# Kernel optimization log

Measured on AMD Instinct MI355X. Metric: run time of the kernel, lower is better.

The kernel has to match this reference:

```python
import jax, jax.numpy as jnp
import numpy as np

N_NODES = 50000


def _gcn_norm(edge_index):
    # symmetric GCN normalization 1/sqrt(deg_src*deg_dst), computed from edge list
    src, dst = edge_index[0], edge_index[1]
    ones = jnp.ones(src.shape[0], dtype=jnp.float32)
    deg = jax.ops.segment_sum(ones, dst, num_segments=N_NODES)
    deg = jnp.maximum(deg, 1.0)
    inv_sqrt = jax.lax.rsqrt(deg)
    return inv_sqrt[src] * inv_sqrt[dst]  # [E]


def _graph_conv(x, src, dst, norm, W, b):
    # gather messages from source nodes, normalize, scatter-add to destinations
    msgs = x[src] * norm[:, None]                       # [E, F]
    agg = jax.ops.segment_sum(msgs, dst, num_segments=N_NODES)  # [N, F]
    return agg @ W + b


def setup_inputs() -> dict:
    key = jax.random.key(0)
    ks = jax.random.split(key, 8)
    F, H, C, E = 128, 256, 40, 600000
    x = jax.random.normal(ks[0], (N_NODES, F), dtype=jnp.float32)
    edge_index = jax.random.randint(ks[1], (2, E), 0, N_NODES, dtype=jnp.int32)
    W1 = jax.random.normal(ks[2], (F, H), dtype=jnp.float32) * (1.0 / np.sqrt(F))
    b1 = jnp.zeros((H,), dtype=jnp.float32)
    W2 = jax.random.normal(ks[3], (H, H), dtype=jnp.float32) * (1.0 / np.sqrt(H))
    b2 = jnp.zeros((H,), dtype=jnp.float32)
    Wd = jax.random.normal(ks[4], (H, C), dtype=jnp.float32) * (1.0 / np.sqrt(H))
    bd = jnp.zeros((C,), dtype=jnp.float32)
    return {"x": x, "edge_index": edge_index, "W1": W1, "b1": b1,
            "W2": W2, "b2": b2, "Wd": Wd, "bd": bd}


def reference(x, edge_index, W1, b1, W2, b2, Wd, bd):
    src, dst = edge_index[0], edge_index[1]
    norm = _gcn_norm(edge_index)
    h = jax.nn.relu(_graph_conv(x, src, dst, norm, W1, b1))
    h = jax.nn.relu(_graph_conv(h, src, dst, norm, W2, b2))
    return jax.nn.softmax(h @ Wd + bd, axis=-1)
```

## Files before the change

kernel.cpp:

```cpp
#include <hip/hip_runtime.h>
#include <hip/hip_bf16.h>
#include <math.h>

#define N_NODES 50000

typedef short short8 __attribute__((ext_vector_type(8)));
typedef float f32x4 __attribute__((ext_vector_type(4)));

static __device__ __forceinline__ void split2(float x, unsigned short& hi, unsigned short& lo) {
    unsigned u = __builtin_bit_cast(unsigned, x);
    unsigned r = u + 0x7FFF + ((u >> 16) & 1);
    hi = (unsigned short)(r >> 16);
    float hf = __builtin_bit_cast(float, (unsigned)hi << 16);
    float res = x - hf;
    unsigned v = __builtin_bit_cast(unsigned, res);
    unsigned r2 = v + 0x7FFF + ((v >> 16) & 1);
    lo = (unsigned short)(r2 >> 16);
}


__global__ void deg_kernel(const int* __restrict__ dst, int* __restrict__ deg, int E) {
    int e = blockIdx.x * blockDim.x + threadIdx.x;
    if (e < E) atomicAdd(&deg[dst[e]], 1);
}


__global__ void scan_p1(const int* __restrict__ deg, int* __restrict__ bsum, int n) {
    int t = threadIdx.x;
    int base = blockIdx.x * 1024 + t * 4;
    int4 v = make_int4(0, 0, 0, 0);
    if (base + 3 < n) v = *(const int4*)(deg + base);
    else {
        if (base + 0 < n) v.x = deg[base + 0];
        if (base + 1 < n) v.y = deg[base + 1];
        if (base + 2 < n) v.z = deg[base + 2];
    }
    int s = v.x + v.y + v.z + v.w;
    #pragma unroll
    for (int off = 32; off > 0; off >>= 1) s += __shfl_xor(s, off);
    __shared__ int wpart[4];
    if ((t & 63) == 0) wpart[t >> 6] = s;
    __syncthreads();
    if (t == 0) bsum[blockIdx.x] = wpart[0] + wpart[1] + wpart[2] + wpart[3];
}

__global__ void scan_p2(int* __restrict__ bsum, int nb, int* __restrict__ rowptr, int n) {
    int t = threadIdx.x;
    int v = (t < nb) ? bsum[t] : 0;
    int sc = v;
    #pragma unroll
    for (int off = 1; off < 64; off <<= 1) {
        int u = __shfl_up(sc, off);
        if (t >= off) sc += u;
    }
    if (t < nb) bsum[t] = sc - v;
    if (t == 63) rowptr[n] = sc;
}

__global__ void scan_p3(const int* __restrict__ deg, const int* __restrict__ bsum,
                        int* __restrict__ rowptr, int* __restrict__ cursor,
                        float* __restrict__ inv, int n) {
    int t = threadIdx.x;
    int base = blockIdx.x * 1024 + t * 4;
    int4 v = make_int4(0, 0, 0, 0);
    if (base + 3 < n) v = *(const int4*)(deg + base);
    else {
        if (base + 0 < n) v.x = deg[base + 0];
        if (base + 1 < n) v.y = deg[base + 1];
        if (base + 2 < n) v.z = deg[base + 2];
    }
    int s = v.x + v.y + v.z + v.w;
    int lane = t & 63;
    int sc = s;
    #pragma unroll
    for (int off = 1; off < 64; off <<= 1) {
        int u = __shfl_up(sc, off);
        if (lane >= off) sc += u;
    }
    __shared__ int wpart[4], woff[4];
    if (lane == 63) wpart[t >> 6] = sc;
    __syncthreads();
    if (t == 0) { int a = 0; for (int i = 0; i < 4; ++i) { woff[i] = a; a += wpart[i]; } }
    __syncthreads();
    int run = bsum[blockIdx.x] + woff[t >> 6] + (sc - s);
    if (base + 0 < n) { rowptr[base + 0] = run; cursor[base + 0] = run; run += v.x; inv[base + 0] = rsqrtf(fmaxf((float)v.x, 1.0f)); }
    if (base + 1 < n) { rowptr[base + 1] = run; cursor[base + 1] = run; run += v.y; inv[base + 1] = rsqrtf(fmaxf((float)v.y, 1.0f)); }
    if (base + 2 < n) { rowptr[base + 2] = run; cursor[base + 2] = run; run += v.z; inv[base + 2] = rsqrtf(fmaxf((float)v.z, 1.0f)); }
    if (base + 3 < n) { rowptr[base + 3] = run; cursor[base + 3] = run; run += v.w; inv[base + 3] = rsqrtf(fmaxf((float)v.w, 1.0f)); }
}


__global__ void fill_kernel(const int* __restrict__ src, const int* __restrict__ dst,
                            const float* __restrict__ inv, int* __restrict__ cursor,
                            int* __restrict__ src_s, float* __restrict__ norm_s, int E) {
    int e = blockIdx.x * blockDim.x + threadIdx.x;
    if (e >= E) return;
    int s = src[e];
    int d = dst[e];
    int pos = atomicAdd(&cursor[d], 1);
    src_s[pos] = s;
    norm_s[pos] = inv[s] * inv[d];
}


__global__ void gather_agg_pass(const float* __restrict__ x, int coff, int ss,
                                const int* __restrict__ rowptr, const int* __restrict__ src_s,
                                const float* __restrict__ norm_s,
                                unsigned short* __restrict__ agg_hi,
                                unsigned short* __restrict__ agg_lo, int as) {
    int node = blockIdx.x * 4 + (threadIdx.x >> 6);
    if (node >= N_NODES) return;
    int lane = threadIdx.x & 63;
    int beg = rowptr[node];
    int end = rowptr[node + 1];
    const float* xb = x + coff + (size_t)lane * 2;

    float2 acc = {0.0f, 0.0f};
    int p = beg;
    for (; p + 4 <= end; p += 4) {
        int s0 = src_s[p], s1 = src_s[p + 1], s2 = src_s[p + 2], s3 = src_s[p + 3];
        float n0 = norm_s[p], n1 = norm_s[p + 1], n2 = norm_s[p + 2], n3 = norm_s[p + 3];
        float2 v0 = *(const float2*)(xb + (size_t)s0 * ss);
        float2 v1 = *(const float2*)(xb + (size_t)s1 * ss);
        float2 v2 = *(const float2*)(xb + (size_t)s2 * ss);
        float2 v3 = *(const float2*)(xb + (size_t)s3 * ss);
        acc.x = fmaf(v0.x, n0, acc.x); acc.y = fmaf(v0.y, n0, acc.y);
        acc.x = fmaf(v1.x, n1, acc.x); acc.y = fmaf(v1.y, n1, acc.y);
        acc.x = fmaf(v2.x, n2, acc.x); acc.y = fmaf(v2.y, n2, acc.y);
        acc.x = fmaf(v3.x, n3, acc.x); acc.y = fmaf(v3.y, n3, acc.y);
    }
    for (; p < end; ++p) {
        int s0 = src_s[p];
        float n0 = norm_s[p];
        float2 v0 = *(const float2*)(xb + (size_t)s0 * ss);
        acc.x = fmaf(v0.x, n0, acc.x);
        acc.y = fmaf(v0.y, n0, acc.y);
    }

    unsigned short h0, l0, h1, l1;
    split2(acc.x, h0, l0);
    split2(acc.y, h1, l1);
    unsigned hp = (unsigned)h0 | ((unsigned)h1 << 16);
    unsigned lp = (unsigned)l0 | ((unsigned)l1 << 16);
    size_t o = (size_t)node * as + coff + (size_t)lane * 2;
    *(unsigned*)(agg_hi + o) = hp;
    *(unsigned*)(agg_lo + o) = lp;
}


__global__ void split_w_all(const float* __restrict__ W1, const float* __restrict__ W2,
                            unsigned short* __restrict__ w1hi, unsigned short* __restrict__ w1lo,
                            unsigned short* __restrict__ w2hi, unsigned short* __restrict__ w2lo) {
    int i = blockIdx.x * 256 + threadIdx.x;
    if (i < 128 * 256) {
        int k = i >> 8;
        int n = i & 255;
        unsigned short h, l;
        split2(W1[i], h, l);
        w1hi[(size_t)n * 128 + k] = h;
        w1lo[(size_t)n * 128 + k] = l;
    } else {
        int j = i - 128 * 256;
        int k = j >> 8;
        int n = j & 255;
        unsigned short h, l;
        split2(W2[j], h, l);
        w2hi[(size_t)n * 256 + k] = h;
        w2lo[(size_t)n * 256 + k] = l;
    }
}


template<int K, bool RELU>
__global__ __launch_bounds__(256) void gemm_mfma_kernel(
    const unsigned short* __restrict__ Ahi, const unsigned short* __restrict__ Alo,
    const unsigned short* __restrict__ Bhi, const unsigned short* __restrict__ Blo,
    const float* __restrict__ bias, float* __restrict__ out, int M)
{
    constexpr int LDA = 40;
    __shared__ unsigned short AsH[2][32][LDA];
    __shared__ unsigned short AsL[2][32][LDA];

    int tid = threadIdx.x;
    int lane = tid & 63;
    int wave = tid >> 6;
    int row0 = blockIdx.x * 32;
    int col0 = wave * 64;
    int lr = lane & 15;
    int lhi = lane >> 4;
    int koff0 = lhi * 8;

    int s = tid & 127;
    int srow = s >> 2;
    int skg = (s & 3) << 3;
    const unsigned short* Astage = (tid < 128) ? Ahi : Alo;

    f32x4 acc[4][2];
    #pragma unroll
    for (int i = 0; i < 4; ++i)
        #pragma unroll
        for (int j = 0; j < 2; ++j) acc[i][j] = (f32x4){0.f, 0.f, 0.f, 0.f};

    short8 rstage;
    rstage = *(const short8*)(Astage + (size_t)(row0 + srow) * K + skg);
    if (tid < 128) *(short8*)&AsH[0][srow][skg] = rstage;
    else           *(short8*)&AsL[0][srow][skg] = rstage;
    __syncthreads();

    constexpr int NT = K / 32;
    #pragma unroll 1
    for (int t = 0; t < NT; ++t) {
        int cur = t & 1;
        int ko = t * 32 + koff0;

        short8 bh[4], bl[4];
        #pragma unroll
        for (int cf = 0; cf < 4; ++cf) {
            size_t boff = (size_t)(col0 + cf * 16 + lr) * K + ko;
            bh[cf] = *(const short8*)(Bhi + boff);
            bl[cf] = *(const short8*)(Blo + boff);
        }

        if (t + 1 < NT) {
            rstage = *(const short8*)(Astage + (size_t)(row0 + srow) * K + (t + 1) * 32 + skg);
        }

        short8 ah[2], al[2];
        #pragma unroll
        for (int rf = 0; rf < 2; ++rf) {
            ah[rf] = *(const short8*)&AsH[cur][rf * 16 + lr][koff0];
            al[rf] = *(const short8*)&AsL[cur][rf * 16 + lr][koff0];
        }

        #pragma unroll
        for (int cf = 0; cf < 4; ++cf)
            #pragma unroll
            for (int rf = 0; rf < 2; ++rf) {
                acc[cf][rf] = __builtin_amdgcn_mfma_f32_16x16x32_bf16(bh[cf], ah[rf], acc[cf][rf], 0, 0, 0);
                acc[cf][rf] = __builtin_amdgcn_mfma_f32_16x16x32_bf16(bl[cf], ah[rf], acc[cf][rf], 0, 0, 0);
                acc[cf][rf] = __builtin_amdgcn_mfma_f32_16x16x32_bf16(bh[cf], al[rf], acc[cf][rf], 0, 0, 0);
            }

        if (t + 1 < NT) {
            if (tid < 128) *(short8*)&AsH[cur ^ 1][srow][skg] = rstage;
            else           *(short8*)&AsL[cur ^ 1][srow][skg] = rstage;
        }
        __syncthreads();
    }

    #pragma unroll
    for (int cf = 0; cf < 4; ++cf) {
        int c = col0 + cf * 16 + lhi * 4;
        float4 bv = *(const float4*)(bias + c);
        #pragma unroll
        for (int rf = 0; rf < 2; ++rf) {
            int r = row0 + rf * 16 + lr;
            if (r < M) {
                float4 v;
                v.x = acc[cf][rf][0] + bv.x;
                v.y = acc[cf][rf][1] + bv.y;
                v.z = acc[cf][rf][2] + bv.z;
                v.w = acc[cf][rf][3] + bv.w;
                if (RELU) {
                    v.x = fmaxf(v.x, 0.f); v.y = fmaxf(v.y, 0.f);
                    v.z = fmaxf(v.z, 0.f); v.w = fmaxf(v.w, 0.f);
                }
                *(float4*)(out + (size_t)r * 256 + c) = v;
            }
        }
    }
}


__global__ __launch_bounds__(256) void dense_softmax_kernel(const float* __restrict__ h,
                                                            const float* __restrict__ Wd,
                                                            const float* __restrict__ bd,
                                                            float* __restrict__ out, int M) {
    __shared__ float hs[32][260];
    __shared__ float wt[40][260];
    int tid = threadIdx.x;
    int row0 = blockIdx.x * 32;

    for (int i = tid; i < 40 * 256; i += 256) {
        int k = i / 40;
        int c = i - k * 40;
        wt[c][k] = Wd[i];
    }
    #pragma unroll
    for (int i = 0; i < 8; ++i) {
        int f = tid + i * 256;
        int r = f >> 6;
        int k4 = (f & 63) << 2;
        float4 v = make_float4(0.f, 0.f, 0.f, 0.f);
        if (row0 + r < M) v = *(const float4*)(h + (size_t)(row0 + r) * 256 + k4);
        *(float4*)&hs[r][k4] = v;
    }
    __syncthreads();

    int r  = tid >> 3;
    int cg = tid & 7;
    int c0 = cg * 5;

    float acc[5] = {0.f, 0.f, 0.f, 0.f, 0.f};
    #pragma unroll 4
    for (int k4 = 0; k4 < 64; ++k4) {
        float4 hv = *(float4*)&hs[r][k4 * 4];
        #pragma unroll
        for (int j = 0; j < 5; ++j) {
            float4 wv = *(float4*)&wt[c0 + j][k4 * 4];
            acc[j] = fmaf(hv.x, wv.x, acc[j]);
            acc[j] = fmaf(hv.y, wv.y, acc[j]);
            acc[j] = fmaf(hv.z, wv.z, acc[j]);
            acc[j] = fmaf(hv.w, wv.w, acc[j]);
        }
    }
    #pragma unroll
    for (int j = 0; j < 5; ++j) acc[j] += bd[c0 + j];

    float m = acc[0];
    #pragma unroll
    for (int j = 1; j < 5; ++j) m = fmaxf(m, acc[j]);
    #pragma unroll
    for (int off = 1; off < 8; off <<= 1) m = fmaxf(m, __shfl_xor(m, off));

    float e[5], s = 0.f;
    #pragma unroll
    for (int j = 0; j < 5; ++j) { e[j] = expf(acc[j] - m); s += e[j]; }
    #pragma unroll
    for (int off = 1; off < 8; off <<= 1) s += __shfl_xor(s, off);

    int row = row0 + r;
    if (row < M) {
        float inv_s = 1.0f / s;
        float* orow = out + (size_t)row * 40 + c0;
        #pragma unroll
        for (int j = 0; j < 5; ++j) orow[j] = e[j] * inv_s;
    }
}


extern "C" void kernel_launch(void* const* d_in, const int* in_sizes, int n_in,
                              void* d_out, int out_size, void* d_ws, size_t ws_size,
                              hipStream_t stream) {
    const float* x  = (const float*)d_in[0];
    const int*   ei = (const int*)d_in[1];
    const float* W1 = (const float*)d_in[2];
    const float* b1 = (const float*)d_in[3];
    const float* W2 = (const float*)d_in[4];
    const float* b2 = (const float*)d_in[5];
    const float* Wd = (const float*)d_in[6];
    const float* bd = (const float*)d_in[7];
    float* out = (float*)d_out;

    const int N = N_NODES;
    const int E = in_sizes[1] / 2;
    const int* src = ei;
    const int* dst = ei + E;

    const int MP = 50048;

    char* ws = (char*)d_ws;
    size_t off = 0;
    auto alloc = [&](size_t bytes) { char* p = ws + off; off += (bytes + 1023) & ~(size_t)1023; return p; };
    int*   deg    = (int*)alloc((size_t)N * 4);
    float* inv    = (float*)alloc((size_t)N * 4);
    int*   rowptr = (int*)alloc((size_t)(N + 1) * 4);
    int*   cursor = (int*)alloc((size_t)N * 4);
    int*   bsum   = (int*)alloc((size_t)64 * 4);
    int*   src_s  = (int*)alloc((size_t)E * 4);
    float* norm_s = (float*)alloc((size_t)E * 4);
    float* h1     = (float*)alloc((size_t)N * 256 * 4);
    unsigned short* aggU = (unsigned short*)alloc((size_t)MP * 256 * 2 * 2);
    unsigned short* w1hi = (unsigned short*)alloc((size_t)128 * 256 * 2);
    unsigned short* w1lo = (unsigned short*)alloc((size_t)128 * 256 * 2);
    unsigned short* w2hi = (unsigned short*)alloc((size_t)256 * 256 * 2);
    unsigned short* w2lo = (unsigned short*)alloc((size_t)256 * 256 * 2);

    unsigned short* agg1_hi = aggU;
    unsigned short* agg1_lo = aggU + (size_t)MP * 128;
    unsigned short* agg2_hi = aggU;
    unsigned short* agg2_lo = aggU + (size_t)MP * 256;
    float* h2 = h1;

    hipMemsetAsync(deg, 0, (size_t)N * 4, stream);

    const int nb = (N + 1023) / 1024;

    deg_kernel<<<(E + 255) / 256, 256, 0, stream>>>(dst, deg, E);
    scan_p1<<<nb, 256, 0, stream>>>(deg, bsum, N);
    scan_p2<<<1, 64, 0, stream>>>(bsum, nb, rowptr, N);
    scan_p3<<<nb, 256, 0, stream>>>(deg, bsum, rowptr, cursor, inv, N);
    fill_kernel<<<(E + 255) / 256, 256, 0, stream>>>(src, dst, inv, cursor, src_s, norm_s, E);

    split_w_all<<<(128 * 256 + 256 * 256) / 256, 256, 0, stream>>>(W1, W2, w1hi, w1lo, w2hi, w2lo);

    const int gblocks = (N + 3) / 4;

    gather_agg_pass<<<gblocks, 256, 0, stream>>>(x, 0, 128, rowptr, src_s, norm_s, agg1_hi, agg1_lo, 128);
    gemm_mfma_kernel<128, true><<<MP / 32, 256, 0, stream>>>(agg1_hi, agg1_lo, w1hi, w1lo, b1, h1, N);

    gather_agg_pass<<<gblocks, 256, 0, stream>>>(h1, 0,   256, rowptr, src_s, norm_s, agg2_hi, agg2_lo, 256);
    gather_agg_pass<<<gblocks, 256, 0, stream>>>(h1, 128, 256, rowptr, src_s, norm_s, agg2_hi, agg2_lo, 256);
    gemm_mfma_kernel<256, true><<<MP / 32, 256, 0, stream>>>(agg2_hi, agg2_lo, w2hi, w2lo, b2, h2, N);

    dense_softmax_kernel<<<(N + 31) / 32, 256, 0, stream>>>(h2, Wd, bd, out, N);
}
```

Before: 357.4 us.

## Fuse sparse gather-aggregation into MFMA GEMM via shared-memory staging

Replaces the separate gather/aggregate passes and the GEMM kernels with one fused kernel per layer. Each block aggregates the neighbor features of its 32 nodes, splits them into bf16 hi/lo and writes them straight into shared memory, then runs the MFMA GEMM from LDS without the double-buffered global staging or per-tile syncs. This removes the global round trip of the aggregated hi/lo buffers and several launches. In exchange each wave gathers 8 nodes serially with less unrolling (2 instead of 4), the gather phase may expose more latency, and h2 now gets its own buffer.

```diff
diff --git a/kernel.cpp b/kernel.cpp
--- a/kernel.cpp
+++ b/kernel.cpp
@@ -100,51 +100,6 @@
     int pos = atomicAdd(&cursor[d], 1);
     src_s[pos] = s;
     norm_s[pos] = inv[s] * inv[d];
-}
-
-
-__global__ void gather_agg_pass(const float* __restrict__ x, int coff, int ss,
-                                const int* __restrict__ rowptr, const int* __restrict__ src_s,
-                                const float* __restrict__ norm_s,
-                                unsigned short* __restrict__ agg_hi,
-                                unsigned short* __restrict__ agg_lo, int as) {
-    int node = blockIdx.x * 4 + (threadIdx.x >> 6);
-    if (node >= N_NODES) return;
-    int lane = threadIdx.x & 63;
-    int beg = rowptr[node];
-    int end = rowptr[node + 1];
-    const float* xb = x + coff + (size_t)lane * 2;
-
-    float2 acc = {0.0f, 0.0f};
-    int p = beg;
-    for (; p + 4 <= end; p += 4) {
-        int s0 = src_s[p], s1 = src_s[p + 1], s2 = src_s[p + 2], s3 = src_s[p + 3];
-        float n0 = norm_s[p], n1 = norm_s[p + 1], n2 = norm_s[p + 2], n3 = norm_s[p + 3];
-        float2 v0 = *(const float2*)(xb + (size_t)s0 * ss);
-        float2 v1 = *(const float2*)(xb + (size_t)s1 * ss);
-        float2 v2 = *(const float2*)(xb + (size_t)s2 * ss);
-        float2 v3 = *(const float2*)(xb + (size_t)s3 * ss);
-        acc.x = fmaf(v0.x, n0, acc.x); acc.y = fmaf(v0.y, n0, acc.y);
-        acc.x = fmaf(v1.x, n1, acc.x); acc.y = fmaf(v1.y, n1, acc.y);
-        acc.x = fmaf(v2.x, n2, acc.x); acc.y = fmaf(v2.y, n2, acc.y);
-        acc.x = fmaf(v3.x, n3, acc.x); acc.y = fmaf(v3.y, n3, acc.y);
-    }
-    for (; p < end; ++p) {
-        int s0 = src_s[p];
-        float n0 = norm_s[p];
-        float2 v0 = *(const float2*)(xb + (size_t)s0 * ss);
-        acc.x = fmaf(v0.x, n0, acc.x);
-        acc.y = fmaf(v0.y, n0, acc.y);
-    }
-
-    unsigned short h0, l0, h1, l1;
-    split2(acc.x, h0, l0);
-    split2(acc.y, h1, l1);
-    unsigned hp = (unsigned)h0 | ((unsigned)h1 << 16);
-    unsigned lp = (unsigned)l0 | ((unsigned)l1 << 16);
-    size_t o = (size_t)node * as + coff + (size_t)lane * 2;
-    *(unsigned*)(agg_hi + o) = hp;
-    *(unsigned*)(agg_lo + o) = lp;
 }
 
 
@@ -172,66 +127,116 @@
 
 
 template<int K, bool RELU>
-__global__ __launch_bounds__(256) void gemm_mfma_kernel(
-    const unsigned short* __restrict__ Ahi, const unsigned short* __restrict__ Alo,
-    const unsigned short* __restrict__ Bhi, const unsigned short* __restrict__ Blo,
+__global__ __launch_bounds__(256) void fused_conv_kernel(
+    const float* __restrict__ X,
+    const int* __restrict__ rowptr, const int* __restrict__ src_s,
+    const float* __restrict__ norm_s,
+    const unsigned short* __restrict__ Whi, const unsigned short* __restrict__ Wlo,
     const float* __restrict__ bias, float* __restrict__ out, int M)
 {
-    constexpr int LDA = 40;
-    __shared__ unsigned short AsH[2][32][LDA];
-    __shared__ unsigned short AsL[2][32][LDA];
+    constexpr int NT = K / 32;
+    constexpr int CH = 32 * 40 + 8;
+    __shared__ unsigned short AsH[NT][CH];
+    __shared__ unsigned short AsL[NT][CH];
 
     int tid = threadIdx.x;
     int lane = tid & 63;
     int wave = tid >> 6;
     int row0 = blockIdx.x * 32;
+
+    for (int i = 0; i < 8; ++i) {
+        int r = wave * 8 + i;
+        int node = row0 + r;
+        if (node >= M) break;
+        int beg = rowptr[node], end = rowptr[node + 1];
+
+        if constexpr (K == 128) {
+            const float* xb = X + (size_t)lane * 2;
+            float2 acc = {0.f, 0.f};
+            int p = beg;
+            for (; p + 2 <= end; p += 2) {
+                int s0 = src_s[p], s1 = src_s[p + 1];
+                float n0 = norm_s[p], n1 = norm_s[p + 1];
+                float2 v0 = *(const float2*)(xb + (size_t)s0 * K);
+                float2 v1 = *(const float2*)(xb + (size_t)s1 * K);
+                acc.x = fmaf(v0.x, n0, acc.x); acc.y = fmaf(v0.y, n0, acc.y);
+                acc.x = fmaf(v1.x, n1, acc.x); acc.y = fmaf(v1.y, n1, acc.y);
+            }
+            if (p < end) {
+                int s0 = src_s[p];
+                float n0 = norm_s[p];
+                float2 v0 = *(const float2*)(xb + (size_t)s0 * K);
+                acc.x = fmaf(v0.x, n0, acc.x); acc.y = fmaf(v0.y, n0, acc.y);
+            }
+            unsigned short h0, l0, h1, l1;
+            split2(acc.x, h0, l0);
+            split2(acc.y, h1, l1);
+            int c = lane >> 4;
+            int e = r * 40 + ((lane & 15) << 1);
+            *(ushort2*)&AsH[c][e] = make_ushort2(h0, h1);
+            *(ushort2*)&AsL[c][e] = make_ushort2(l0, l1);
+        } else {
+            const float* xb = X + (size_t)lane * 4;
+            float4 acc = {0.f, 0.f, 0.f, 0.f};
+            int p = beg;
+            for (; p + 2 <= end; p += 2) {
+                int s0 = src_s[p], s1 = src_s[p + 1];
+                float n0 = norm_s[p], n1 = norm_s[p + 1];
+                float4 v0 = *(const float4*)(xb + (size_t)s0 * K);
+                float4 v1 = *(const float4*)(xb + (size_t)s1 * K);
+                acc.x = fmaf(v0.x, n0, acc.x); acc.y = fmaf(v0.y, n0, acc.y);
+                acc.z = fmaf(v0.z, n0, acc.z); acc.w = fmaf(v0.w, n0, acc.w);
+                acc.x = fmaf(v1.x, n1, acc.x); acc.y = fmaf(v1.y, n1, acc.y);
+                acc.z = fmaf(v1.z, n1, acc.z); acc.w = fmaf(v1.w, n1, acc.w);
+            }
+            if (p < end) {
+                int s0 = src_s[p];
+                float n0 = norm_s[p];
+                float4 v0 = *(const float4*)(xb + (size_t)s0 * K);
+                acc.x = fmaf(v0.x, n0, acc.x); acc.y = fmaf(v0.y, n0, acc.y);
+                acc.z = fmaf(v0.z, n0, acc.z); acc.w = fmaf(v0.w, n0, acc.w);
+            }
+            unsigned short h0, l0, h1, l1, h2, l2, h3, l3;
+            split2(acc.x, h0, l0);
+            split2(acc.y, h1, l1);
+            split2(acc.z, h2, l2);
+            split2(acc.w, h3, l3);
+            int c = lane >> 3;
+            int e = r * 40 + ((lane & 7) << 2);
+            *(ushort4*)&AsH[c][e] = make_ushort4(h0, h1, h2, h3);
+            *(ushort4*)&AsL[c][e] = make_ushort4(l0, l1, l2, l3);
+        }
+    }
+    __syncthreads();
+
     int col0 = wave * 64;
     int lr = lane & 15;
     int lhi = lane >> 4;
     int koff0 = lhi * 8;
 
-    int s = tid & 127;
-    int srow = s >> 2;
-    int skg = (s & 3) << 3;
-    const unsigned short* Astage = (tid < 128) ? Ahi : Alo;
-
     f32x4 acc[4][2];
     #pragma unroll
     for (int i = 0; i < 4; ++i)
         #pragma unroll
         for (int j = 0; j < 2; ++j) acc[i][j] = (f32x4){0.f, 0.f, 0.f, 0.f};
 
-    short8 rstage;
-    rstage = *(const short8*)(Astage + (size_t)(row0 + srow) * K + skg);
-    if (tid < 128) *(short8*)&AsH[0][srow][skg] = rstage;
-    else           *(short8*)&AsL[0][srow][skg] = rstage;
-    __syncthreads();
-
-    constexpr int NT = K / 32;
-    #pragma unroll 1
+    #pragma unroll 2
     for (int t = 0; t < NT; ++t) {
-        int cur = t & 1;
         int ko = t * 32 + koff0;
-
         short8 bh[4], bl[4];
         #pragma unroll
         for (int cf = 0; cf < 4; ++cf) {
             size_t boff = (size_t)(col0 + cf * 16 + lr) * K + ko;
-            bh[cf] = *(const short8*)(Bhi + boff);
-            bl[cf] = *(const short8*)(Blo + boff);
-        }
-
-        if (t + 1 < NT) {
-            rstage = *(const short8*)(Astage + (size_t)(row0 + srow) * K + (t + 1) * 32 + skg);
-        }
-
+            bh[cf] = *(const short8*)(Whi + boff);
+            bl[cf] = *(const short8*)(Wlo + boff);
+        }
         short8 ah[2], al[2];
         #pragma unroll
         for (int rf = 0; rf < 2; ++rf) {
-            ah[rf] = *(const short8*)&AsH[cur][rf * 16 + lr][koff0];
-            al[rf] = *(const short8*)&AsL[cur][rf * 16 + lr][koff0];
-        }
-
+            int e = (rf * 16 + lr) * 40 + koff0;
+            ah[rf] = *(const short8*)&AsH[t][e];
+            al[rf] = *(const short8*)&AsL[t][e];
+        }
         #pragma unroll
         for (int cf = 0; cf < 4; ++cf)
             #pragma unroll
@@ -240,12 +245,6 @@
                 acc[cf][rf] = __builtin_amdgcn_mfma_f32_16x16x32_bf16(bl[cf], ah[rf], acc[cf][rf], 0, 0, 0);
                 acc[cf][rf] = __builtin_amdgcn_mfma_f32_16x16x32_bf16(bh[cf], al[rf], acc[cf][rf], 0, 0, 0);
             }
-
-        if (t + 1 < NT) {
-            if (tid < 128) *(short8*)&AsH[cur ^ 1][srow][skg] = rstage;
-            else           *(short8*)&AsL[cur ^ 1][srow][skg] = rstage;
-        }
-        __syncthreads();
     }
 
     #pragma unroll
@@ -357,8 +356,6 @@
     const int* src = ei;
     const int* dst = ei + E;
 
-    const int MP = 50048;
-
     char* ws = (char*)d_ws;
     size_t off = 0;
     auto alloc = [&](size_t bytes) { char* p = ws + off; off += (bytes + 1023) & ~(size_t)1023; return p; };
@@ -370,17 +367,11 @@
     int*   src_s  = (int*)alloc((size_t)E * 4);
     float* norm_s = (float*)alloc((size_t)E * 4);
     float* h1     = (float*)alloc((size_t)N * 256 * 4);
-    unsigned short* aggU = (unsigned short*)alloc((size_t)MP * 256 * 2 * 2);
+    float* h2     = (float*)alloc((size_t)N * 256 * 4);
     unsigned short* w1hi = (unsigned short*)alloc((size_t)128 * 256 * 2);
     unsigned short* w1lo = (unsigned short*)alloc((size_t)128 * 256 * 2);
     unsigned short* w2hi = (unsigned short*)alloc((size_t)256 * 256 * 2);
     unsigned short* w2lo = (unsigned short*)alloc((size_t)256 * 256 * 2);
-
-    unsigned short* agg1_hi = aggU;
-    unsigned short* agg1_lo = aggU + (size_t)MP * 128;
-    unsigned short* agg2_hi = aggU;
-    unsigned short* agg2_lo = aggU + (size_t)MP * 256;
-    float* h2 = h1;
 
     hipMemsetAsync(deg, 0, (size_t)N * 4, stream);
 
@@ -394,14 +385,13 @@
 
     split_w_all<<<(128 * 256 + 256 * 256) / 256, 256, 0, stream>>>(W1, W2, w1hi, w1lo, w2hi, w2lo);
 
-    const int gblocks = (N + 3) / 4;
-
-    gather_agg_pass<<<gblocks, 256, 0, stream>>>(x, 0, 128, rowptr, src_s, norm_s, agg1_hi, agg1_lo, 128);
-    gemm_mfma_kernel<128, true><<<MP / 32, 256, 0, stream>>>(agg1_hi, agg1_lo, w1hi, w1lo, b1, h1, N);
-
-    gather_agg_pass<<<gblocks, 256, 0, stream>>>(h1, 0,   256, rowptr, src_s, norm_s, agg2_hi, agg2_lo, 256);
-    gather_agg_pass<<<gblocks, 256, 0, stream>>>(h1, 128, 256, rowptr, src_s, norm_s, agg2_hi, agg2_lo, 256);
-    gemm_mfma_kernel<256, true><<<MP / 32, 256, 0, stream>>>(agg2_hi, agg2_lo, w2hi, w2lo, b2, h2, N);
+    const int cblocks = (N + 31) / 32;
+
+    fused_conv_kernel<128, true><<<cblocks, 256, 0, stream>>>(
+        x, rowptr, src_s, norm_s, w1hi, w1lo, b1, h1, N);
+
+    fused_conv_kernel<256, true><<<cblocks, 256, 0, stream>>>(
+        h1, rowptr, src_s, norm_s, w2hi, w2lo, b2, h2, N);
 
     dense_softmax_kernel<<<(N + 31) / 32, 256, 0, stream>>>(h2, Wd, bd, out, N);
 }
```

Result: slower. 406.5 us (+13.7%).

## Preload full A tile into LDS and register-prefetch B fragments in MFMA GEMM

Applied to the files above, without the earlier changes.

The GEMM kernel now loads the block's whole 32-row A slice (all K) into shared memory once, with a single barrier, instead of double-buffering one 32-wide K chunk per iteration with a barrier each step. The K loop is fully unrolled and the B hi/lo fragments for the next step are prefetched into registers while the current MFMAs run. This removes per-iteration barriers and hides global-load latency for B, at the cost of larger LDS (up to 40KB for K=256) and more registers, which may reduce occupancy.

```diff
diff --git a/kernel.cpp b/kernel.cpp
--- a/kernel.cpp
+++ b/kernel.cpp
@@ -177,23 +177,44 @@
     const unsigned short* __restrict__ Bhi, const unsigned short* __restrict__ Blo,
     const float* __restrict__ bias, float* __restrict__ out, int M)
 {
-    constexpr int LDA = 40;
-    __shared__ unsigned short AsH[2][32][LDA];
-    __shared__ unsigned short AsL[2][32][LDA];
+    constexpr int NT = K / 32;
+    constexpr int ROWS = 32;
+    __shared__ unsigned short AsH[NT][ROWS][40];
+    __shared__ unsigned short AsL[NT][ROWS][40];
 
     int tid = threadIdx.x;
     int lane = tid & 63;
     int wave = tid >> 6;
-    int row0 = blockIdx.x * 32;
+    int row0 = blockIdx.x * ROWS;
     int col0 = wave * 64;
     int lr = lane & 15;
     int lhi = lane >> 4;
     int koff0 = lhi * 8;
 
+    constexpr int SLOTS = ROWS * K / 8;
+    constexpr int PER = SLOTS / 128;
+    const unsigned short* Asrc = (tid < 128) ? Ahi : Alo;
     int s = tid & 127;
-    int srow = s >> 2;
-    int skg = (s & 3) << 3;
-    const unsigned short* Astage = (tid < 128) ? Ahi : Alo;
+
+    short8 rr[PER];
+    #pragma unroll
+    for (int j = 0; j < PER; ++j) {
+        int i = j * 128 + s;
+        int row = i / (K / 8);
+        int kg = (i % (K / 8)) * 8;
+        rr[j] = *(const short8*)(Asrc + (size_t)(row0 + row) * K + kg);
+    }
+    #pragma unroll
+    for (int j = 0; j < PER; ++j) {
+        int i = j * 128 + s;
+        int row = i / (K / 8);
+        int kg = (i % (K / 8)) * 8;
+        int c = kg >> 5;
+        int o = kg & 31;
+        if (tid < 128) *(short8*)&AsH[c][row][o] = rr[j];
+        else           *(short8*)&AsL[c][row][o] = rr[j];
+    }
+    __syncthreads();
 
     f32x4 acc[4][2];
     #pragma unroll
@@ -201,37 +222,31 @@
         #pragma unroll
         for (int j = 0; j < 2; ++j) acc[i][j] = (f32x4){0.f, 0.f, 0.f, 0.f};
 
-    short8 rstage;
-    rstage = *(const short8*)(Astage + (size_t)(row0 + srow) * K + skg);
-    if (tid < 128) *(short8*)&AsH[0][srow][skg] = rstage;
-    else           *(short8*)&AsL[0][srow][skg] = rstage;
-    __syncthreads();
-
-    constexpr int NT = K / 32;
-    #pragma unroll 1
+    short8 bh[4], bl[4], bh2[4], bl2[4];
+    #pragma unroll
+    for (int cf = 0; cf < 4; ++cf) {
+        size_t boff = (size_t)(col0 + cf * 16 + lr) * K + koff0;
+        bh[cf] = *(const short8*)(Bhi + boff);
+        bl[cf] = *(const short8*)(Blo + boff);
+    }
+
+    #pragma unroll
     for (int t = 0; t < NT; ++t) {
-        int cur = t & 1;
-        int ko = t * 32 + koff0;
-
-        short8 bh[4], bl[4];
-        #pragma unroll
-        for (int cf = 0; cf < 4; ++cf) {
-            size_t boff = (size_t)(col0 + cf * 16 + lr) * K + ko;
-            bh[cf] = *(const short8*)(Bhi + boff);
-            bl[cf] = *(const short8*)(Blo + boff);
+        if (t + 1 < NT) {
+            int ko = (t + 1) * 32 + koff0;
+            #pragma unroll
+            for (int cf = 0; cf < 4; ++cf) {
+                size_t boff = (size_t)(col0 + cf * 16 + lr) * K + ko;
+                bh2[cf] = *(const short8*)(Bhi + boff);
+                bl2[cf] = *(const short8*)(Blo + boff);
+            }
         }
-
-        if (t + 1 < NT) {
-            rstage = *(const short8*)(Astage + (size_t)(row0 + srow) * K + (t + 1) * 32 + skg);
+        short8 ah[2], al[2];
+        #pragma unroll
+        for (int rf = 0; rf < 2; ++rf) {
+            ah[rf] = *(const short8*)&AsH[t][rf * 16 + lr][koff0];
+            al[rf] = *(const short8*)&AsL[t][rf * 16 + lr][koff0];
         }
-
-        short8 ah[2], al[2];
-        #pragma unroll
-        for (int rf = 0; rf < 2; ++rf) {
-            ah[rf] = *(const short8*)&AsH[cur][rf * 16 + lr][koff0];
-            al[rf] = *(const short8*)&AsL[cur][rf * 16 + lr][koff0];
-        }
-
         #pragma unroll
         for (int cf = 0; cf < 4; ++cf)
             #pragma unroll
@@ -240,12 +255,10 @@
                 acc[cf][rf] = __builtin_amdgcn_mfma_f32_16x16x32_bf16(bl[cf], ah[rf], acc[cf][rf], 0, 0, 0);
                 acc[cf][rf] = __builtin_amdgcn_mfma_f32_16x16x32_bf16(bh[cf], al[rf], acc[cf][rf], 0, 0, 0);
             }
-
         if (t + 1 < NT) {
-            if (tid < 128) *(short8*)&AsH[cur ^ 1][srow][skg] = rstage;
-            else           *(short8*)&AsL[cur ^ 1][srow][skg] = rstage;
+            #pragma unroll
+            for (int cf = 0; cf < 4; ++cf) { bh[cf] = bh2[cf]; bl[cf] = bl2[cf]; }
         }
-        __syncthreads();
     }
 
     #pragma unroll
```

Result: no change. 363.5 us (+1.7%).
